# Optimization experiments

Hardware: AMD Instinct MI355X
Metric: run time of the kernel (lower is better)

## Reference

```python
import jax, jax.numpy as jnp
import numpy as np


def setup_inputs() -> dict:
    key = jax.random.key(0)
    k1, k2 = jax.random.split(key)
    B, M, N, D = 8, 2048, 2048, 1024
    x = jax.random.normal(k1, (B, M, D), dtype=jnp.float32)
    y = jax.random.normal(k2, (B, N, D), dtype=jnp.float32)
    return {"x": x, "y": y}


def reference(x, y):
    # scores e[b,m,n] = <x[b,m], y[b,n]>   (K.batch_dot(x, y, axes=2))
    e = jnp.einsum('bmd,bnd->bmn', x, y)
    # stable softmax over last axis (the exp/max/sum sequence in the original)
    p = jax.nn.softmax(e, axis=-1)
    # K.batch_dot(z, x, axes=1): contract axis 1 (m) of both -> [B, n, d]; V = x
    out = jnp.einsum('bmn,bmd->bnd', p, x)
    return out
```

## Files before the change

### kernel.cpp

```cpp
#include <hip/hip_runtime.h>
#include <hip/hip_bf16.h>
#include <stdint.h>

#define B_ 8
#define M_ 2048
#define N_ 2048
#define D_ 1024

typedef __bf16 bf16x8 __attribute__((ext_vector_type(8)));
typedef float f32x4 __attribute__((ext_vector_type(4)));
typedef uint16_t us4 __attribute__((ext_vector_type(4)));
typedef uint16_t us8 __attribute__((ext_vector_type(8)));

__device__ __forceinline__ uint16_t f2b(float f) {
    uint32_t u = __float_as_uint(f);
    return (uint16_t)((u + 0x7FFFu + ((u >> 16) & 1u)) >> 16);
}
__device__ __forceinline__ float b2f(uint16_t h) {
    return __uint_as_float(((uint32_t)h) << 16);
}

__device__ __forceinline__ void gld16(const uint16_t* g, const uint16_t* l) {
    __builtin_amdgcn_global_load_lds(
        (const __attribute__((address_space(1))) uint32_t*)g,
        (__attribute__((address_space(3))) uint32_t*)l,
        16, 0, 0);
}

__global__ __launch_bounds__(256) void k_split(const float* __restrict__ x,
                                               const float* __restrict__ y,
                                               uint16_t* __restrict__ xh, uint16_t* __restrict__ xl,
                                               uint16_t* __restrict__ yh, uint16_t* __restrict__ yl) {
    const int i = (blockIdx.x * 256 + threadIdx.x) * 4;
    float4 vx = *(const float4*)(x + i);
    float4 vy = *(const float4*)(y + i);
    float fx[4] = {vx.x, vx.y, vx.z, vx.w};
    float fy[4] = {vy.x, vy.y, vy.z, vy.w};
    us4 hx, lx, hy, ly;
#pragma unroll
    for (int k = 0; k < 4; ++k) {
        uint16_t h = f2b(fx[k]);
        hx[k] = h; lx[k] = f2b(fx[k] - b2f(h));
        uint16_t g = f2b(fy[k]);
        hy[k] = g; ly[k] = f2b(fy[k] - b2f(g));
    }
    *(us4*)(xh + i) = hx;
    *(us4*)(xl + i) = lx;
    *(us4*)(yh + i) = hy;
    *(us4*)(yl + i) = ly;
}

#define SBAR0 __builtin_amdgcn_sched_barrier(0)
#define LD8(off) (*(const bf16x8*)&lds[off])
#define RDB(bo)                                                        \
    _Pragma("unroll") for (int j = 0; j < 4; ++j) {                    \
        bh[j] = LD8((bo) + bbase + j * 512);                           \
        bl[j] = LD8((bo) + bbase + 8192 + j * 512);                    \
    }
#define RDA(H, L, bo, q)                                               \
    H[0] = LD8((bo) + abase + ((q)*2) * 512);                          \
    H[1] = LD8((bo) + abase + ((q)*2 + 1) * 512);                      \
    L[0] = LD8((bo) + abase + 8192 + ((q)*2) * 512);                   \
    L[1] = LD8((bo) + abase + 8192 + ((q)*2 + 1) * 512);
#define MMQ(H, L, q)                                                   \
    __builtin_amdgcn_s_setprio(1);                                     \
    _Pragma("unroll") for (int ii = 0; ii < 2; ++ii)                   \
    _Pragma("unroll") for (int j = 0; j < 4; ++j) {                    \
        acc[(q)*2 + ii][j] = __builtin_amdgcn_mfma_f32_16x16x32_bf16(  \
            H[ii], bh[j], acc[(q)*2 + ii][j], 0, 0, 0);                \
        acc[(q)*2 + ii][j] = __builtin_amdgcn_mfma_f32_16x16x32_bf16(  \
            H[ii], bl[j], acc[(q)*2 + ii][j], 0, 0, 0);                \
        acc[(q)*2 + ii][j] = __builtin_amdgcn_mfma_f32_16x16x32_bf16(  \
            L[ii], bh[j], acc[(q)*2 + ii][j], 0, 0, 0);                \
    }                                                                  \
    __builtin_amdgcn_s_setprio(0);

__global__ __launch_bounds__(512, 2) void k_gemm1(const uint16_t* __restrict__ xh,
                                                  const uint16_t* __restrict__ xl,
                                                  const uint16_t* __restrict__ yh,
                                                  const uint16_t* __restrict__ yl,
                                                  float* __restrict__ e,
                                                  float* __restrict__ pmax,
                                                  float* __restrict__ psum) {
    const int b = blockIdx.z;
    const int m0 = blockIdx.x * 256;
    const int n0 = blockIdx.y * 256;
    __shared__ __align__(16) uint16_t lds[65536];

    const int tid = threadIdx.x;
    const int lane = tid & 63;
    const int wid = tid >> 6;
    const int wm = (wid >> 2) * 128;
    const int wn = (wid & 3) * 64;
    const int quad = lane >> 4;
    const int r16 = lane & 15;
    const int swz8 = (quad ^ ((r16 >> 1) & 3)) * 8;

    const int base_row = wid * 16 + (lane >> 2);
    const int gd8 = ((lane & 3) ^ ((lane >> 3) & 3)) * 8;
    const uint16_t* gp[4];
    gp[0] = xh + ((size_t)b * M_ + m0 + base_row) * D_ + gd8;
    gp[1] = xl + ((size_t)b * M_ + m0 + base_row) * D_ + gd8;
    gp[2] = yh + ((size_t)b * N_ + n0 + base_row) * D_ + gd8;
    gp[3] = yl + ((size_t)b * N_ + n0 + base_row) * D_ + gd8;
    const int ldsW = wid * 512;

    const int abase = (wm + r16) * 32 + swz8;
    const int bbase = 16384 + (wn + r16) * 32 + swz8;

    auto STAGE = [&](int dst, int ktn) {
#pragma unroll
        for (int c = 0; c < 8; ++c)
            gld16(gp[c >> 1] + (size_t)(c & 1) * (128 * D_) + ktn * 32,
                  &lds[dst + c * 4096 + ldsW]);
    };

    f32x4 acc[8][4];
#pragma unroll
    for (int i = 0; i < 8; ++i)
#pragma unroll
        for (int j = 0; j < 4; ++j) acc[i][j] = (f32x4){0.f, 0.f, 0.f, 0.f};

    bf16x8 bh[4], bl[4];
    bf16x8 a0h[2], a0l[2];
    bf16x8 a1h[2], a1l[2];

    STAGE(0, 0);
    asm volatile("s_waitcnt vmcnt(0)" ::: "memory");
    SBAR0; __builtin_amdgcn_s_barrier(); SBAR0;
    RDB(0); RDA(a0h, a0l, 0, 0);

    for (int t = 0; t < 32; ++t) {
        const int bo = (t & 1) << 15;
        const int nbo = bo ^ 32768;
        const bool more = t < 31;

        if (more) STAGE(nbo, t + 1);
        RDA(a1h, a1l, bo, 1);
        SBAR0;
        MMQ(a0h, a0l, 0);
        SBAR0;

        RDA(a0h, a0l, bo, 2);
        SBAR0;
        MMQ(a1h, a1l, 1);
        SBAR0;

        RDA(a1h, a1l, bo, 3);
        SBAR0;
        MMQ(a0h, a0l, 2);
        SBAR0;

        asm volatile("s_waitcnt vmcnt(0)" ::: "memory");
        SBAR0; __builtin_amdgcn_s_barrier(); SBAR0;

        if (more) { RDA(a0h, a0l, nbo, 0); }
        SBAR0;
        MMQ(a1h, a1l, 3);
        SBAR0;
        if (more) {
            RDB(nbo);
            SBAR0; __builtin_amdgcn_s_barrier(); SBAR0;
        }
    }

    float* eb = e + (size_t)b * M_ * N_;
    const int grows = (int)gridDim.z * M_;
    const int growbase = b * M_ + m0 + wm;
    const int nb = (n0 + wn) >> 6;
    float* pm = pmax + (size_t)nb * grows + growbase;
    float* ps = psum + (size_t)nb * grows + growbase;

#pragma unroll
    for (int i = 0; i < 8; ++i) {
#pragma unroll
        for (int r = 0; r < 4; ++r) {
            const float v0 = acc[i][0][r], v1 = acc[i][1][r];
            const float v2 = acc[i][2][r], v3 = acc[i][3][r];
            float mrow = fmaxf(fmaxf(v0, v1), fmaxf(v2, v3));
#pragma unroll
            for (int s = 1; s < 16; s <<= 1) mrow = fmaxf(mrow, __shfl_xor(mrow, s, 64));
            float srow_ = __expf(v0 - mrow) + __expf(v1 - mrow)
                        + __expf(v2 - mrow) + __expf(v3 - mrow);
#pragma unroll
            for (int s = 1; s < 16; s <<= 1) srow_ += __shfl_xor(srow_, s, 64);
            const int lrow = i * 16 + quad * 4 + r;
            if (r16 == 0) { pm[lrow] = mrow; ps[lrow] = srow_; }
            const size_t ebase = (size_t)(m0 + wm + lrow) * N_ + n0 + wn + r16;
#pragma unroll
            for (int j = 0; j < 4; ++j) eb[ebase + j * 16] = acc[i][j][r];
        }
    }
}

__global__ __launch_bounds__(256) void k_combine(const float* __restrict__ pmax,
                                                 const float* __restrict__ psum,
                                                 float* __restrict__ mx,
                                                 float* __restrict__ inv, int rows) {
    const int r = blockIdx.x * 256 + threadIdx.x;
    float m = -3.4e38f;
#pragma unroll
    for (int nb = 0; nb < 32; ++nb) m = fmaxf(m, pmax[(size_t)nb * rows + r]);
    float s = 0.f;
#pragma unroll
    for (int nb = 0; nb < 32; ++nb)
        s += psum[(size_t)nb * rows + r] * __expf(pmax[(size_t)nb * rows + r] - m);
    mx[r] = m;
    inv[r] = 1.0f / s;
}

__global__ __launch_bounds__(256) void k_texp(const float* __restrict__ e,
                                              const float* __restrict__ mx,
                                              const float* __restrict__ inv,
                                              uint16_t* __restrict__ pT) {
    const int b = blockIdx.z, m0 = blockIdx.x * 64, n0 = blockIdx.y * 64;
    __shared__ float tile[64 * 65];
    const int t = threadIdx.x;
    const float* eb = e + (size_t)b * M_ * N_;
#pragma unroll
    for (int q = 0; q < 4; ++q) {
        const int row = q * 16 + (t >> 4);
        const int c4 = (t & 15) * 4;
        float4 v = *(const float4*)&eb[(size_t)(m0 + row) * N_ + n0 + c4];
        const float mv = mx[b * M_ + m0 + row];
        const float iv = inv[b * M_ + m0 + row];
        tile[row * 65 + c4 + 0] = __expf(v.x - mv) * iv;
        tile[row * 65 + c4 + 1] = __expf(v.y - mv) * iv;
        tile[row * 65 + c4 + 2] = __expf(v.z - mv) * iv;
        tile[row * 65 + c4 + 3] = __expf(v.w - mv) * iv;
    }
    __syncthreads();
    uint16_t* pb = pT + (size_t)b * N_ * M_;
#pragma unroll
    for (int q = 0; q < 2; ++q) {
        const int n = q * 32 + (t >> 3);
        const int mc = (t & 7) * 8;
        us8 o;
#pragma unroll
        for (int k = 0; k < 8; ++k) o[k] = f2b(tile[(mc + k) * 65 + n]);
        *(us8*)&pb[(size_t)(n0 + n) * M_ + m0 + mc] = o;
    }
}

__global__ __launch_bounds__(256) void k_tx(const float* __restrict__ x,
                                            uint16_t* __restrict__ xt) {
    const int b = blockIdx.z, m0 = blockIdx.x * 64, d0 = blockIdx.y * 64;
    __shared__ float tile[64 * 65];
    const int t = threadIdx.x;
    const float* xb = x + (size_t)b * M_ * D_;
#pragma unroll
    for (int q = 0; q < 4; ++q) {
        const int row = q * 16 + (t >> 4);
        const int c4 = (t & 15) * 4;
        float4 v = *(const float4*)&xb[(size_t)(m0 + row) * D_ + d0 + c4];
        tile[row * 65 + c4 + 0] = v.x;
        tile[row * 65 + c4 + 1] = v.y;
        tile[row * 65 + c4 + 2] = v.z;
        tile[row * 65 + c4 + 3] = v.w;
    }
    __syncthreads();
    uint16_t* xtb = xt + (size_t)b * D_ * M_;
#pragma unroll
    for (int q = 0; q < 2; ++q) {
        const int d = q * 32 + (t >> 3);
        const int mc = (t & 7) * 8;
        us8 o;
#pragma unroll
        for (int k = 0; k < 8; ++k) o[k] = f2b(tile[(mc + k) * 65 + d]);
        *(us8*)&xtb[(size_t)(d0 + d) * M_ + m0 + mc] = o;
    }
}

__global__ __launch_bounds__(256) void k_gemm2(const uint16_t* __restrict__ pT,
                                               const uint16_t* __restrict__ xt,
                                               float* __restrict__ out) {
    const int b = blockIdx.z;
    const int n0 = blockIdx.x * 128;
    const int d0 = blockIdx.y * 128;
    __shared__ __align__(16) uint16_t lds[16384];

    const int tid = threadIdx.x;
    const int lane = tid & 63;
    const int wid = tid >> 6;
    const int wn = (wid & 1) * 64;
    const int wd = (wid >> 1) * 64;
    const int quad = lane >> 4;
    const int r16 = lane & 15;

    const uint16_t* srcA = pT + ((size_t)b * N_ + n0) * M_;
    const uint16_t* srcB = xt + ((size_t)b * D_ + d0) * M_;

    f32x4 acc[4][4];
#pragma unroll
    for (int i = 0; i < 4; ++i)
#pragma unroll
        for (int j = 0; j < 4; ++j) acc[i][j] = (f32x4){0.f, 0.f, 0.f, 0.f};

    for (int kt = 0; kt < M_ / 64; ++kt) {
#pragma unroll
        for (int c = 0; c < 8; ++c) {
            const int offbase = c * 2048 + wid * 512;
            const int tile = offbase >> 13;
            const int o = (offbase & 8191) + lane * 8;
            const int row = o >> 6;
            const int gp = (o & 63) >> 3;
            const int gd = gp ^ (row & 7);
            const uint16_t* sp = tile ? srcB : srcA;
            gld16(sp + (size_t)row * M_ + kt * 64 + gd * 8, &lds[offbase]);
        }
        __syncthreads();

#pragma unroll
        for (int h = 0; h < 2; ++h) {
            const int p = (h * 4 + quad) ^ (r16 & 7);
            bf16x8 a[4], bbr[4];
#pragma unroll
            for (int i = 0; i < 4; ++i) {
                a[i]   = *(const bf16x8*)&lds[(wn + i * 16 + r16) * 64 + p * 8];
                bbr[i] = *(const bf16x8*)&lds[8192 + (wd + i * 16 + r16) * 64 + p * 8];
            }
#pragma unroll
            for (int i = 0; i < 4; ++i)
#pragma unroll
                for (int j = 0; j < 4; ++j)
                    acc[i][j] = __builtin_amdgcn_mfma_f32_16x16x32_bf16(a[i], bbr[j], acc[i][j], 0, 0, 0);
        }
        __syncthreads();
    }

    float* ob = out + (size_t)b * N_ * D_;
#pragma unroll
    for (int i = 0; i < 4; ++i) {
        const int rbase = n0 + wn + i * 16 + quad * 4;
#pragma unroll
        for (int j = 0; j < 4; ++j) {
            const int col = d0 + wd + j * 16 + r16;
#pragma unroll
            for (int r = 0; r < 4; ++r)
                ob[(size_t)(rbase + r) * D_ + col] = acc[i][j][r];
        }
    }
}

extern "C" void kernel_launch(void* const* d_in, const int* in_sizes, int n_in,
                              void* d_out, int out_size, void* d_ws, size_t ws_size,
                              hipStream_t stream) {
    const float* x = (const float*)d_in[0];
    const float* y = (const float*)d_in[1];
    float* out = (float*)d_out;
    char* ws = (char*)d_ws;

    const size_t MiB = 1024 * 1024;
    int g = 8;
    while (g > 1 && (size_t)g * 32 * MiB > ws_size) g >>= 1;
    if ((size_t)g * 32 * MiB > ws_size) return;

    const size_t T = (size_t)g * M_ * D_ * 2;
    uint16_t* xh = (uint16_t*)(ws + 0 * T);
    uint16_t* xl = (uint16_t*)(ws + 1 * T);
    uint16_t* yh = (uint16_t*)(ws + 2 * T);
    uint16_t* yl = (uint16_t*)(ws + 3 * T);
    float*    e  = (float*)(ws + 4 * T);
    float*    mx = (float*)(ws);
    float*    inv = mx + (size_t)g * M_;
    uint16_t* xt = xl;
    uint16_t* pT = yh;

    const size_t pelems = (size_t)32 * g * M_;
    float* pmax = (float*)d_out + (size_t)B_ * N_ * D_ - 2 * pelems;
    float* psum = pmax + pelems;

    for (int c0 = 0; c0 < B_; c0 += g) {
        const float* xc = x + (size_t)c0 * M_ * D_;
        const float* yc = y + (size_t)c0 * N_ * D_;
        float* oc = out + (size_t)c0 * N_ * D_;

        hipLaunchKernelGGL(k_split, dim3((g * M_ * D_) / (256 * 4)), dim3(256), 0, stream,
                           xc, yc, xh, xl, yh, yl);
        hipLaunchKernelGGL(k_gemm1, dim3(M_ / 256, N_ / 256, g), dim3(512), 0, stream,
                           xh, xl, yh, yl, e, pmax, psum);
        hipLaunchKernelGGL(k_combine, dim3((g * M_) / 256), dim3(256), 0, stream,
                           pmax, psum, mx, inv, g * M_);
        hipLaunchKernelGGL(k_texp, dim3(M_ / 64, N_ / 64, g), dim3(256), 0, stream,
                           e, mx, inv, pT);
        hipLaunchKernelGGL(k_tx, dim3(M_ / 64, D_ / 64, g), dim3(256), 0, stream, xc, xt);
        hipLaunchKernelGGL(k_gemm2, dim3(N_ / 128, D_ / 128, g), dim3(256), 0, stream,
                           pT, xt, oc);
    }
}
```

Measured before the change: 498.9 us.

## Double-buffer LDS in second GEMM and transpose from bf16 copy of x

The second GEMM now uses two LDS buffers, so the async global-to-LDS loads for the next K tile are issued while MFMAs run on the current tile. This hides load latency but doubles LDS use per block, which can lower occupancy. The x transpose kernel now reads the already-rounded bf16 high part of x instead of the fp32 input, roughly halving its read traffic. To keep that bf16 buffer intact, the softmax max and inverse-sum arrays move from the workspace start into the tail of the output buffer.

```diff
diff --git a/kernel.cpp b/kernel.cpp
--- a/kernel.cpp
+++ b/kernel.cpp
@@ -242,21 +242,19 @@
     }
 }
 
-__global__ __launch_bounds__(256) void k_tx(const float* __restrict__ x,
+__global__ __launch_bounds__(256) void k_tx(const uint16_t* __restrict__ xh,
                                             uint16_t* __restrict__ xt) {
     const int b = blockIdx.z, m0 = blockIdx.x * 64, d0 = blockIdx.y * 64;
     __shared__ float tile[64 * 65];
     const int t = threadIdx.x;
-    const float* xb = x + (size_t)b * M_ * D_;
-#pragma unroll
-    for (int q = 0; q < 4; ++q) {
-        const int row = q * 16 + (t >> 4);
-        const int c4 = (t & 15) * 4;
-        float4 v = *(const float4*)&xb[(size_t)(m0 + row) * D_ + d0 + c4];
-        tile[row * 65 + c4 + 0] = v.x;
-        tile[row * 65 + c4 + 1] = v.y;
-        tile[row * 65 + c4 + 2] = v.z;
-        tile[row * 65 + c4 + 3] = v.w;
+    const uint16_t* xb = xh + (size_t)b * M_ * D_;
+#pragma unroll
+    for (int q = 0; q < 2; ++q) {
+        const int row = q * 32 + (t >> 3);
+        const int c8 = (t & 7) * 8;
+        us8 v = *(const us8*)&xb[(size_t)(m0 + row) * D_ + d0 + c8];
+#pragma unroll
+        for (int k = 0; k < 8; ++k) tile[row * 65 + c8 + k] = b2f(v[k]);
     }
     __syncthreads();
     uint16_t* xtb = xt + (size_t)b * D_ * M_;
@@ -277,7 +275,7 @@
     const int b = blockIdx.z;
     const int n0 = blockIdx.x * 128;
     const int d0 = blockIdx.y * 128;
-    __shared__ __align__(16) uint16_t lds[16384];
+    __shared__ __align__(16) uint16_t lds[32768];
 
     const int tid = threadIdx.x;
     const int lane = tid & 63;
@@ -296,7 +294,7 @@
 #pragma unroll
         for (int j = 0; j < 4; ++j) acc[i][j] = (f32x4){0.f, 0.f, 0.f, 0.f};
 
-    for (int kt = 0; kt < M_ / 64; ++kt) {
+    auto STAGE = [&](int dst, int kt) {
 #pragma unroll
         for (int c = 0; c < 8; ++c) {
             const int offbase = c * 2048 + wid * 512;
@@ -306,9 +304,17 @@
             const int gp = (o & 63) >> 3;
             const int gd = gp ^ (row & 7);
             const uint16_t* sp = tile ? srcB : srcA;
-            gld16(sp + (size_t)row * M_ + kt * 64 + gd * 8, &lds[offbase]);
-        }
-        __syncthreads();
+            gld16(sp + (size_t)row * M_ + kt * 64 + gd * 8, &lds[dst + offbase]);
+        }
+    };
+
+    STAGE(0, 0);
+    __syncthreads();
+
+    for (int kt = 0; kt < M_ / 64; ++kt) {
+        const int bo = (kt & 1) << 14;
+        const int nbo = bo ^ 16384;
+        if (kt < M_ / 64 - 1) STAGE(nbo, kt + 1);
 
 #pragma unroll
         for (int h = 0; h < 2; ++h) {
@@ -316,8 +322,8 @@
             bf16x8 a[4], bbr[4];
 #pragma unroll
             for (int i = 0; i < 4; ++i) {
-                a[i]   = *(const bf16x8*)&lds[(wn + i * 16 + r16) * 64 + p * 8];
-                bbr[i] = *(const bf16x8*)&lds[8192 + (wd + i * 16 + r16) * 64 + p * 8];
+                a[i]   = *(const bf16x8*)&lds[bo + (wn + i * 16 + r16) * 64 + p * 8];
+                bbr[i] = *(const bf16x8*)&lds[bo + 8192 + (wd + i * 16 + r16) * 64 + p * 8];
             }
 #pragma unroll
             for (int i = 0; i < 4; ++i)
@@ -361,14 +367,15 @@
     uint16_t* yh = (uint16_t*)(ws + 2 * T);
     uint16_t* yl = (uint16_t*)(ws + 3 * T);
     float*    e  = (float*)(ws + 4 * T);
-    float*    mx = (float*)(ws);
-    float*    inv = mx + (size_t)g * M_;
     uint16_t* xt = xl;
     uint16_t* pT = yh;
 
     const size_t pelems = (size_t)32 * g * M_;
-    float* pmax = (float*)d_out + (size_t)B_ * N_ * D_ - 2 * pelems;
+    float* dtail = (float*)d_out + (size_t)B_ * N_ * D_;
+    float* pmax = dtail - 2 * pelems;
     float* psum = pmax + pelems;
+    float* mx   = dtail - 2 * pelems - 2 * (size_t)g * M_;
+    float* inv  = mx + (size_t)g * M_;
 
     for (int c0 = 0; c0 < B_; c0 += g) {
         const float* xc = x + (size_t)c0 * M_ * D_;
@@ -383,7 +390,7 @@
                            pmax, psum, mx, inv, g * M_);
         hipLaunchKernelGGL(k_texp, dim3(M_ / 64, N_ / 64, g), dim3(256), 0, stream,
                            e, mx, inv, pT);
-        hipLaunchKernelGGL(k_tx, dim3(M_ / 64, D_ / 64, g), dim3(256), 0, stream, xc, xt);
+        hipLaunchKernelGGL(k_tx, dim3(M_ / 64, D_ / 64, g), dim3(256), 0, stream, xh, xt);
         hipLaunchKernelGGL(k_gemm2, dim3(N_ / 128, D_ / 128, g), dim3(256), 0, stream,
                            pT, xt, oc);
     }
```

New measurement: 467.6 us. 6.3% less time.
